# Kernel optimization log

Measured on AMD Instinct MI355X. Metric: run time of the kernel, lower is better.

Reference implementation:

```python
import jax, jax.numpy as jnp
import numpy as np

K = 16          # gcn_k
NHEAD = 4
C = 256         # feat_dims
EPS = 1e-5
LAYERS = ('gcn', 'cross_attn', 'gcn', 'cross_attn')


def _inorm(x, axes):
    # torch InstanceNorm (affine=False): normalize per (batch, channel) over spatial axes
    mu = jnp.mean(x, axes, keepdims=True)
    var = jnp.var(x, axes, keepdims=True)
    return (x - mu) * jax.lax.rsqrt(var + EPS)


def _lrelu(x):
    return jnp.where(x >= 0, x, 0.2 * x)


def _conv1d(x, W, b=None):
    # 1x1 Conv1d: x (B,Cin,N), W (Cout,Cin)
    y = jnp.einsum('bcn,oc->bon', x, W)
    return y if b is None else y + b[None, :, None]


def _graph_features(feats, coords, k):
    # feats (B,N,Cf), coords (B,N,3) -> (B,N,k,2Cf)  [EdgeConv features]
    sq = jnp.sum(coords * coords, axis=-1)  # (B,N)
    d = sq[:, :, None] + sq[:, None, :] - 2.0 * jnp.einsum('bnc,bmc->bnm', coords, coords)
    _, inds = jax.lax.top_k(-d, k + 1)       # k+1 smallest distances, sorted
    inds = inds[:, :, 1:]                    # drop self
    neigh = jax.vmap(lambda f, i: f[i])(feats, inds)  # (B,N,k,Cf)
    center = jnp.broadcast_to(feats[:, :, None, :], neigh.shape)
    return jnp.concatenate([center, neigh - center], axis=-1)


def _gcn(coords, feats, W1, W2, W3, k):
    # coords (B,3,N), feats (B,C,N) -> (B,C,N)
    c = jnp.transpose(coords, (0, 2, 1))
    f = jnp.transpose(feats, (0, 2, 1))
    g1 = _graph_features(f, c, k)                                   # (B,N,k,2C)
    h1 = _lrelu(_inorm(jnp.einsum('bnkc,oc->bonk', g1, W1), (2, 3)))
    f1 = jnp.max(h1, axis=-1)                                       # (B,C,N)
    g2 = _graph_features(jnp.transpose(f1, (0, 2, 1)), c, k)        # (B,N,k,2C)
    h2 = _lrelu(_inorm(jnp.einsum('bnkc,oc->bonk', g2, W2), (2, 3)))
    f2 = jnp.max(h2, axis=-1)                                       # (B,2C,N)
    f3 = jnp.concatenate([feats, f1, f2], axis=1)                   # (B,4C,N)
    return _lrelu(_inorm(_conv1d(f3, W3), (2,)))


def _cross_attn(f1, f2, Wq, bq, Wk, bk, Wv, bv, Wo, bo, Wm1, bm1, Wm2, bm2, nhead):
    B, Cc, N = f1.shape
    d = Cc // nhead
    # torch reshape (B, C, N) -> (B, d, nhead, N): channel c = dd*nhead + h
    q = _conv1d(f1, Wq, bq).reshape(B, d, nhead, -1)
    k = _conv1d(f2, Wk, bk).reshape(B, d, nhead, -1)
    v = _conv1d(f2, Wv, bv).reshape(B, d, nhead, -1)
    scores = jnp.einsum('bdhn,bdhm->bhnm', q, k) / (d ** 0.5)
    attn = jax.nn.softmax(scores, axis=-1)
    feats = jnp.einsum('bhnm,bdhm->bdhn', attn, v).reshape(B, Cc, -1)
    feats = _conv1d(feats, Wo, bo)
    h = _conv1d(jnp.concatenate([f1, feats], axis=1), Wm1, bm1)
    h = jax.nn.relu(_inorm(h, (2,)))
    return _conv1d(h, Wm2, bm2)


def _forward(coords1, feats1, coords2, feats2, gcn_W1, gcn_W2, gcn_W3, ca):
    for li, name in enumerate(LAYERS):
        i = li // 2  # index into stacked per-block params
        if name == 'gcn':
            feats1 = _gcn(coords1, feats1, gcn_W1[i], gcn_W2[i], gcn_W3[i], K)
            feats2 = _gcn(coords2, feats2, gcn_W1[i], gcn_W2[i], gcn_W3[i], K)
        else:
            p = tuple(t[i] for t in ca)
            feats1 = _cross_attn(feats1, feats2, *p, NHEAD)
            feats2 = _cross_attn(feats2, feats1, *p, NHEAD)
    return feats1, feats2


def setup_inputs() -> dict:
    key = jax.random.key(0)
    ks = jax.random.split(key, 20)
    B, N, M = 2, 2048, 2048
    s = 0.05
    f32 = jnp.float32
    return {
        'coords1': jax.random.normal(ks[0], (B, 3, N), f32),
        'feats1': jax.random.normal(ks[1], (B, C, N), f32),
        'coords2': jax.random.normal(ks[2], (B, 3, M), f32),
        'feats2': jax.random.normal(ks[3], (B, C, M), f32),
        'gcn_W1': jax.random.normal(ks[4], (2, C, 2 * C), f32) * s,
        'gcn_W2': jax.random.normal(ks[5], (2, 2 * C, 2 * C), f32) * s,
        'gcn_W3': jax.random.normal(ks[6], (2, C, 4 * C), f32) * s,
        'ca_Wq': jax.random.normal(ks[7], (2, C, C), f32) * s,
        'ca_bq': jax.random.normal(ks[8], (2, C), f32) * s,
        'ca_Wk': jax.random.normal(ks[9], (2, C, C), f32) * s,
        'ca_bk': jax.random.normal(ks[10], (2, C), f32) * s,
        'ca_Wv': jax.random.normal(ks[11], (2, C, C), f32) * s,
        'ca_bv': jax.random.normal(ks[12], (2, C), f32) * s,
        'ca_Wo': jax.random.normal(ks[13], (2, C, C), f32) * s,
        'ca_bo': jax.random.normal(ks[14], (2, C), f32) * s,
        'ca_Wm1': jax.random.normal(ks[15], (2, 2 * C, 2 * C), f32) * s,
        'ca_bm1': jax.random.normal(ks[16], (2, 2 * C), f32) * s,
        'ca_Wm2': jax.random.normal(ks[17], (2, C, 2 * C), f32) * s,
        'ca_bm2': jax.random.normal(ks[18], (2, C), f32) * s,
    }


def reference(coords1, feats1, coords2, feats2, gcn_W1, gcn_W2, gcn_W3,
              ca_Wq, ca_bq, ca_Wk, ca_bk, ca_Wv, ca_bv, ca_Wo, ca_bo,
              ca_Wm1, ca_bm1, ca_Wm2, ca_bm2):
    ca = (ca_Wq, ca_bq, ca_Wk, ca_bk, ca_Wv, ca_bv, ca_Wo, ca_bo,
          ca_Wm1, ca_bm1, ca_Wm2, ca_bm2)
    return _forward(coords1, feats1, coords2, feats2, gcn_W1, gcn_W2, gcn_W3, ca)
```

## Files before the change

### kernel.cpp

```cpp
#include <hip/hip_runtime.h>


namespace {

constexpr int BB = 2, NPV = 2048, CCH = 256, KNB = 16;
typedef long long i64;
typedef unsigned short u16;
constexpr i64 NSTR  = (i64)NPV * 256;
constexpr i64 NSTR2 = (i64)NPV * 512;
constexpr i64 NSTR4 = (i64)NPV * 1024;
constexpr i64 MB = 1048576;

typedef __attribute__((ext_vector_type(8))) short short8v;
typedef __attribute__((ext_vector_type(4))) float f32x4;

__device__ __forceinline__ float lrelu(float v) { return v >= 0.f ? v : 0.2f * v; }

__device__ __forceinline__ void splitbf(float x, u16& h, u16& l) {
  unsigned u = __float_as_uint(x);
  h = (u16)(u >> 16);
  float hf = __uint_as_float(u & 0xffff0000u);
  l = (u16)(__float_as_uint(x - hf) >> 16);
}

__global__ __launch_bounds__(256) void k_diag(float* out, int n, float v) {
  int i = blockIdx.x * 256 + threadIdx.x;
  if (i < n) out[i] = v;
}

__global__ __launch_bounds__(256) void k_setup(
    const float* __restrict__ fa, const float* __restrict__ fb,
    float* __restrict__ Xa, float* __restrict__ Xb,
    const float* __restrict__ W1b, const float* __restrict__ W2b,
    float* __restrict__ UVS,
    const float* __restrict__ Wob, float* __restrict__ WoT,
    const float* __restrict__ Wm1b_, float* __restrict__ Wfull,
    const float* __restrict__ bm1b_, const float* __restrict__ bob,
    float* __restrict__ bcomb) {
  int blk = blockIdx.x;
  int t = threadIdx.x;
  if (blk < 8192) {
    int gi = blk * 256 + t;
    bool second = gi >= (1 << 20);
    int idx = gi & ((1 << 20) - 1);
    int b = idx >> 19;
    int n = (idx >> 8) & (NPV - 1);
    int c = idx & (CCH - 1);
    const float* f = second ? fb : fa;
    float* X = second ? Xb : Xa;
    X[idx] = f[((i64)b * CCH + c) * NPV + n];
  } else if (blk < 11264) {
    int i = (blk - 8192) * 256 + t;
    int li = i / 393216;
    int r0 = i - li * 393216;
    const float* W1 = W1b + (i64)li * 131072;
    const float* W2 = W2b + (i64)li * 262144;
    float* dst = UVS + (i64)li * 393216;
    if (r0 < 131072) {
      int r = r0 >> 8, c = r0 & 255;
      dst[r0] = (r < 256) ? W1[(i64)r * 512 + c] - W1[(i64)r * 512 + 256 + c]
                          : W1[(i64)(r - 256) * 512 + 256 + c];
    } else {
      int j = r0 - 131072;
      int r = j >> 8, c = j & 255;
      dst[131072 + j] = (r < 512) ? W2[(i64)r * 512 + c] - W2[(i64)r * 512 + 256 + c]
                                  : W2[(i64)(r - 512) * 512 + 256 + c];
    }
  } else if (blk < 11776) {
    int i = (blk - 11264) * 256 + t;
    int li = i >> 16, rem = i & 65535;
    int c = rem >> 8, k = rem & 255;
    WoT[(i64)li * 65536 + c * 256 + k] = Wob[(i64)li * 65536 + k * 256 + c];
  } else if (blk < 12800) {
    int i = (blk - 11776) * 256 + t;
    int li = i >> 17, rem = i & 131071;
    int o = rem >> 8, c = rem & 255;
    Wfull[(i64)li * 262144 + o * 512 + c] = Wm1b_[(i64)li * 262144 + o * 512 + c];
  } else {
    int g = (blk - 12800) * 256 + t;
    int li = g >> 9, o = g & 511;
    const float* wm1 = Wm1b_ + (i64)li * 262144 + (i64)o * 512 + 256;
    const float* bo = bob + (i64)li * 256;
    float acc = bm1b_[(i64)li * 512 + o];
    for (int k = 0; k < 256; k++) acc += wm1[k] * bo[k];
    bcomb[(i64)li * 512 + o] = acc;
  }
}

__global__ __launch_bounds__(256) void k_final2(const float* __restrict__ Xa,
                                                const float* __restrict__ Xb,
                                                float* __restrict__ out) {
  int gi = blockIdx.x * 256 + threadIdx.x;
  bool second = gi >= (1 << 20);
  int idx = gi & ((1 << 20) - 1);
  int b = idx >> 19;
  int c = (idx >> 11) & (CCH - 1);
  int n = idx & (NPV - 1);
  const float* X = second ? Xb : Xa;
  out[gi] = X[((i64)b * NPV + n) * CCH + c];
}

__global__ __launch_bounds__(256) void k_knnp(const float* __restrict__ c1,
                                              const float* __restrict__ c2,
                                              int* __restrict__ o1,
                                              int* __restrict__ o2) {
#pragma clang fp contract(off)
  __shared__ float4 csq[NPV];
  int set = blockIdx.y >> 1, b = blockIdx.y & 1;
  const float* cb = (set ? c2 : c1) + (i64)b * 3 * NPV;
  int* ob = (set ? o2 : o1) + (i64)b * NPV * KNB;
  for (int m = threadIdx.x; m < NPV; m += 256) {
    float x = cb[m], y = cb[NPV + m], z = cb[2 * NPV + m];
    csq[m] = make_float4(x, y, z, x * x + y * y + z * z);
  }
  __syncthreads();
  int w = threadIdx.x >> 6, lane = threadIdx.x & 63;
  int n = blockIdx.x * 4 + w;
  float4 cn = csq[n];
  float xn = cn.x, yn = cn.y, zn = cn.z, sn = cn.w;
  float dc[32];
#pragma unroll
  for (int t = 0; t < 32; t++) {
    float4 c = csq[t * 64 + lane];
    float dot = xn * c.x + yn * c.y + zn * c.z;
    dc[t] = (sn + c.w) - 2.0f * dot;
  }
  float wd = -3.4e38f; int wm = -1;
  int* o = ob + (i64)n * KNB;
  for (int r = 0; r < KNB + 1; r++) {
    float bd = 3.4e38f; int bm = 0x7fffffff;
#pragma unroll
    for (int t = 0; t < 32; t++) {
      int m = t * 64 + lane;
      float d = dc[t];
      bool valid = (d > wd) || (d == wd && m > wm);
      if (valid && (d < bd || (d == bd && m < bm))) { bd = d; bm = m; }
    }
    for (int mask = 1; mask < 64; mask <<= 1) {
      float od = __shfl_xor(bd, mask);
      int om = __shfl_xor(bm, mask);
      if (od < bd || (od == bd && om < bm)) { bd = od; bm = om; }
    }
    if (r > 0 && lane == 0) o[r - 1] = bm & (NPV - 1);
    wd = bd; wm = bm;
  }
}

template <bool ANORM, bool ACAT, bool ESTAT>
__global__ __launch_bounds__(256) void k_gemm(
    const float* __restrict__ A, int lda, i64 sA,
    const float* __restrict__ A2,
    const float* __restrict__ W, int ldw, i64 sW,
    const float* __restrict__ bias,
    float* __restrict__ C, int ldc, i64 sC,
    int K, int mode, int act,
    const float* __restrict__ pin, int nchA, float invA,
    float* __restrict__ pout, int ncolsTot) {
  __shared__ __align__(16) u16 Ah[128][36], Al[128][36], Bh[128][36], Bl[128][36];
  __shared__ float mv[512], rv[512];
  __shared__ float cs[128][2];
  int b = blockIdx.z;
  A += (i64)b * sA;
  if (ACAT) A2 += (i64)b * NSTR;
  C += (i64)b * sC;
  int m0 = blockIdx.x * 128, n0 = blockIdx.y * 128;
  int tid = threadIdx.x;
  int w = tid >> 6, l = tid & 63;
  int wr = w >> 1, wc = w & 1;
  int lc = l & 15, lq = l >> 4;
  int srow = tid >> 1, skh = (tid & 1) * 16;

  if (ANORM) {
    for (int c = tid; c < K; c += 256) {
      float s = 0.f, ss = 0.f;
      for (int hh = 0; hh < nchA; hh++) {
        s  += pin[((i64)(b * nchA + hh) * K + c) * 2];
        ss += pin[((i64)(b * nchA + hh) * K + c) * 2 + 1];
      }
      float mu = s * invA;
      mv[c] = mu;
      rv[c] = 1.0f / sqrtf(ss * invA - mu * mu + 1e-5f);
    }
    __syncthreads();
  }

  const float* Ap = A + (i64)(m0 + srow) * lda + skh;
  const float* Wp = W + (i64)b * sW + (i64)(n0 + srow) * ldw + skh;

  auto loadA = [&](int kt, float4* v) {
#pragma unroll
    for (int j = 0; j < 4; j++) {
      if (ACAT) {
        int col0 = kt + skh;
        const float* ap = (col0 < 256)
            ? A  + (i64)(m0 + srow) * 256 + col0
            : A2 + (i64)(m0 + srow) * 256 + (col0 - 256);
        v[j] = *(const float4*)(ap + j * 4);
      } else {
        v[j] = *(const float4*)(Ap + kt + j * 4);
      }
    }
  };
  auto loadW = [&](int kt, float4* v) {
#pragma unroll
    for (int j = 0; j < 4; j++) v[j] = *(const float4*)(Wp + kt + j * 4);
  };

  float4 ar[4], wv4[4];
  loadA(0, ar); loadW(0, wv4);

  f32x4 acc[4][4];
#pragma unroll
  for (int i = 0; i < 4; i++)
#pragma unroll
    for (int j = 0; j < 4; j++)
#pragma unroll
      for (int r = 0; r < 4; r++) acc[i][j][r] = 0.f;

  int koff = lq * 8;
  for (int kt = 0; kt < K; kt += 32) {
    __syncthreads();
#pragma unroll
    for (int j = 0; j < 4; j++) {
      float4 a = ar[j];
      if (ANORM) {
        float4 mu = *(const float4*)&mv[kt + skh + j * 4];
        float4 rs = *(const float4*)&rv[kt + skh + j * 4];
        a.x = (a.x - mu.x) * rs.x; a.y = (a.y - mu.y) * rs.y;
        a.z = (a.z - mu.z) * rs.z; a.w = (a.w - mu.w) * rs.w;
        if (act == 1) { a.x = lrelu(a.x); a.y = lrelu(a.y);
                        a.z = lrelu(a.z); a.w = lrelu(a.w); }
        else { a.x = fmaxf(a.x, 0.f); a.y = fmaxf(a.y, 0.f);
               a.z = fmaxf(a.z, 0.f); a.w = fmaxf(a.w, 0.f); }
      }
      u16 h0, h1, h2, h3, l0, l1, l2, l3;
      splitbf(a.x, h0, l0); splitbf(a.y, h1, l1);
      splitbf(a.z, h2, l2); splitbf(a.w, h3, l3);
      *(ushort4*)&Ah[srow][skh + j * 4] = make_ushort4(h0, h1, h2, h3);
      *(ushort4*)&Al[srow][skh + j * 4] = make_ushort4(l0, l1, l2, l3);
      float4 bb = wv4[j];
      splitbf(bb.x, h0, l0); splitbf(bb.y, h1, l1);
      splitbf(bb.z, h2, l2); splitbf(bb.w, h3, l3);
      *(ushort4*)&Bh[srow][skh + j * 4] = make_ushort4(h0, h1, h2, h3);
      *(ushort4*)&Bl[srow][skh + j * 4] = make_ushort4(l0, l1, l2, l3);
    }
    __syncthreads();
    if (kt + 32 < K) { loadA(kt + 32, ar); loadW(kt + 32, wv4); }
    short8v ah[4], al4[4], bh[4], bl4[4];
#pragma unroll
    for (int i = 0; i < 4; i++) {
      int r = wr * 64 + i * 16 + lc;
      ah[i]  = *(const short8v*)&Ah[r][koff];
      al4[i] = *(const short8v*)&Al[r][koff];
    }
#pragma unroll
    for (int j = 0; j < 4; j++) {
      int r = wc * 64 + j * 16 + lc;
      bh[j]  = *(const short8v*)&Bh[r][koff];
      bl4[j] = *(const short8v*)&Bl[r][koff];
    }
#pragma unroll
    for (int i = 0; i < 4; i++) {
#pragma unroll
      for (int j = 0; j < 4; j++) {
        acc[i][j] = __builtin_amdgcn_mfma_f32_16x16x32_bf16(ah[i], bh[j], acc[i][j], 0, 0, 0);
        acc[i][j] = __builtin_amdgcn_mfma_f32_16x16x32_bf16(al4[i], bh[j], acc[i][j], 0, 0, 0);
        acc[i][j] = __builtin_amdgcn_mfma_f32_16x16x32_bf16(ah[i], bl4[j], acc[i][j], 0, 0, 0);
      }
    }
  }

  float sj[4] = {0.f, 0.f, 0.f, 0.f}, ssj[4] = {0.f, 0.f, 0.f, 0.f};
#pragma unroll
  for (int j = 0; j < 4; j++) {
    int col = n0 + wc * 64 + j * 16 + lc;
    float bv = (mode == 0 && bias) ? bias[col] : 0.f;
#pragma unroll
    for (int i = 0; i < 4; i++) {
      int rbase = m0 + wr * 64 + i * 16 + lq * 4;
#pragma unroll
      for (int r = 0; r < 4; r++) {
        float* cp = &C[(i64)(rbase + r) * ldc + col];
        float v = acc[i][j][r] + ((mode == 0) ? bv : *cp);
        *cp = v;
        if (ESTAT) { sj[j] += v; ssj[j] += v * v; }
      }
    }
  }
  if (ESTAT) {
#pragma unroll
    for (int j = 0; j < 4; j++) {
      sj[j]  += __shfl_xor(sj[j], 16);  sj[j]  += __shfl_xor(sj[j], 32);
      ssj[j] += __shfl_xor(ssj[j], 16); ssj[j] += __shfl_xor(ssj[j], 32);
    }
    __syncthreads();
    if (wr == 0 && lq == 0) {
#pragma unroll
      for (int j = 0; j < 4; j++) {
        int cl = wc * 64 + j * 16 + lc;
        cs[cl][0] = sj[j]; cs[cl][1] = ssj[j];
      }
    }
    __syncthreads();
    if (wr == 1 && lq == 0) {
#pragma unroll
      for (int j = 0; j < 4; j++) {
        int cl = wc * 64 + j * 16 + lc;
        cs[cl][0] += sj[j]; cs[cl][1] += ssj[j];
      }
    }
    __syncthreads();
    if (tid < 128) {
      i64 slot = ((i64)(b * gridDim.x + blockIdx.x) * ncolsTot + n0 + tid) * 2;
      pout[slot] = cs[tid][0];
      pout[slot + 1] = cs[tid][1];
    }
  }
}

__global__ __launch_bounds__(256) void k_qkv(
    const float* __restrict__ XA, const float* __restrict__ XB,
    const float* __restrict__ Wq, const float* __restrict__ Wk,
    const float* __restrict__ Wv,
    const float* __restrict__ bq, const float* __restrict__ bk,
    const float* __restrict__ bv,
    float* __restrict__ Qp, float* __restrict__ Kp, float* __restrict__ Vp) {
  __shared__ __align__(16) u16 Ah[128][36], Al[128][36], Bh[128][36], Bl[128][36];
  int z = blockIdx.z;
  int mat = z >> 1, b = z & 1;
  const float* A = (mat == 0 ? XA : XB) + (i64)b * NSTR;
  const float* W = (mat == 0 ? Wq : (mat == 1 ? Wk : Wv));
  const float* bias = (mat == 0 ? bq : (mat == 1 ? bk : bv));
  float* C = (mat == 0 ? Qp : (mat == 1 ? Kp : Vp)) + (i64)b * NSTR;
  int m0 = blockIdx.x * 128, n0 = blockIdx.y * 128;
  int tid = threadIdx.x;
  int w = tid >> 6, l = tid & 63;
  int wr = w >> 1, wc = w & 1;
  int lc = l & 15, lq = l >> 4;
  int srow = tid >> 1, skh = (tid & 1) * 16;
  const float* Ap = A + (i64)(m0 + srow) * 256 + skh;
  const float* Wp = W + (i64)(n0 + srow) * 256 + skh;
  float4 ar[4], wv4[4];
#pragma unroll
  for (int j = 0; j < 4; j++) { ar[j] = *(const float4*)(Ap + j * 4);
                                wv4[j] = *(const float4*)(Wp + j * 4); }
  f32x4 acc[4][4];
#pragma unroll
  for (int i = 0; i < 4; i++)
#pragma unroll
    for (int j = 0; j < 4; j++)
#pragma unroll
      for (int r = 0; r < 4; r++) acc[i][j][r] = 0.f;
  int koff = lq * 8;
  for (int kt = 0; kt < 256; kt += 32) {
    __syncthreads();
#pragma unroll
    for (int j = 0; j < 4; j++) {
      u16 h0, h1, h2, h3, l0, l1, l2, l3;
      splitbf(ar[j].x, h0, l0); splitbf(ar[j].y, h1, l1);
      splitbf(ar[j].z, h2, l2); splitbf(ar[j].w, h3, l3);
      *(ushort4*)&Ah[srow][skh + j * 4] = make_ushort4(h0, h1, h2, h3);
      *(ushort4*)&Al[srow][skh + j * 4] = make_ushort4(l0, l1, l2, l3);
      splitbf(wv4[j].x, h0, l0); splitbf(wv4[j].y, h1, l1);
      splitbf(wv4[j].z, h2, l2); splitbf(wv4[j].w, h3, l3);
      *(ushort4*)&Bh[srow][skh + j * 4] = make_ushort4(h0, h1, h2, h3);
      *(ushort4*)&Bl[srow][skh + j * 4] = make_ushort4(l0, l1, l2, l3);
    }
    __syncthreads();
    if (kt + 32 < 256) {
#pragma unroll
      for (int j = 0; j < 4; j++) { ar[j] = *(const float4*)(Ap + kt + 32 + j * 4);
                                    wv4[j] = *(const float4*)(Wp + kt + 32 + j * 4); }
    }
    short8v ah[4], al4[4], bh[4], bl4[4];
#pragma unroll
    for (int i = 0; i < 4; i++) {
      int r = wr * 64 + i * 16 + lc;
      ah[i]  = *(const short8v*)&Ah[r][koff];
      al4[i] = *(const short8v*)&Al[r][koff];
    }
#pragma unroll
    for (int j = 0; j < 4; j++) {
      int r = wc * 64 + j * 16 + lc;
      bh[j]  = *(const short8v*)&Bh[r][koff];
      bl4[j] = *(const short8v*)&Bl[r][koff];
    }
#pragma unroll
    for (int i = 0; i < 4; i++)
#pragma unroll
      for (int j = 0; j < 4; j++) {
        acc[i][j] = __builtin_amdgcn_mfma_f32_16x16x32_bf16(ah[i], bh[j], acc[i][j], 0, 0, 0);
        acc[i][j] = __builtin_amdgcn_mfma_f32_16x16x32_bf16(al4[i], bh[j], acc[i][j], 0, 0, 0);
        acc[i][j] = __builtin_amdgcn_mfma_f32_16x16x32_bf16(ah[i], bl4[j], acc[i][j], 0, 0, 0);
      }
  }
#pragma unroll
  for (int j = 0; j < 4; j++) {
    int col = n0 + wc * 64 + j * 16 + lc;
    float bv = bias[col];
#pragma unroll
    for (int i = 0; i < 4; i++) {
      int rbase = m0 + wr * 64 + i * 16 + lq * 4;
#pragma unroll
      for (int r = 0; r < 4; r++) {
        float v = acc[i][j][r] + bv;
        int row = rbase + r;
        if (mat == 0) C[(i64)row * 256 + col] = v;
        else C[((i64)(col & 3) * 2048 + row) * 64 + (col >> 2)] = v;
      }
    }
  }
}

__global__ __launch_bounds__(256) void k_y3(
    const float* __restrict__ Xbase, const float* __restrict__ F1b,
    const float* __restrict__ F2b, const float* __restrict__ W3b,
    float* __restrict__ Cb,
    const float* __restrict__ pA, const float* __restrict__ pB,
    float* __restrict__ pout, int li) {
  __shared__ __align__(16) u16 Ah[128][36], Al[128][36], Bh[128][36], Bl[128][36];
  __shared__ float mv[1024], rv[1024];
  __shared__ float cs[128][2];
  int z = blockIdx.z;
  const float* X = Xbase + (i64)z * NSTR;
  const float* F1 = F1b + (i64)z * NSTR;
  const float* F2 = F2b + (i64)z * NSTR2;
  const float* W3 = W3b + (i64)li * 262144;
  float* C = Cb + (i64)z * NSTR;
  int m0 = blockIdx.x * 128, n0 = blockIdx.y * 128;
  int tid = threadIdx.x;
  int w = tid >> 6, l = tid & 63;
  int wr = w >> 1, wc = w & 1;
  int lc = l & 15, lq = l >> 4;
  int srow = tid >> 1, skh = (tid & 1) * 16;
  for (int c = tid; c < 768; c += 256) {
    int col = 256 + c;
    const float* P; int cols, idx;
    if (col < 512) { P = pA; cols = 256; idx = col - 256; }
    else           { P = pB; cols = 512; idx = col - 512; }
    float s = 0.f, ss = 0.f;
    for (int hh = 0; hh < 64; hh++) {
      s  += P[((i64)(z * 64 + hh) * cols + idx) * 2];
      ss += P[((i64)(z * 64 + hh) * cols + idx) * 2 + 1];
    }
    float mu = s * (1.f / 32768.f);
    mv[col] = mu;
    rv[col] = 1.0f / sqrtf(ss * (1.f / 32768.f) - mu * mu + 1e-5f);
  }
  __syncthreads();
  auto loadA = [&](int kt, float4* v) {
    int col0 = kt + skh;
    const float* ap;
    if (col0 < 256)      ap = X  + (i64)(m0 + srow) * 256 + col0;
    else if (col0 < 512) ap = F1 + (i64)(m0 + srow) * 256 + (col0 - 256);
    else                 ap = F2 + (i64)(m0 + srow) * 512 + (col0 - 512);
#pragma unroll
    for (int j = 0; j < 4; j++) v[j] = *(const float4*)(ap + j * 4);
  };
  const float* Wp = W3 + (i64)(n0 + srow) * 1024 + skh;
  float4 ar[4], wv4[4];
  loadA(0, ar);
#pragma unroll
  for (int j = 0; j < 4; j++) wv4[j] = *(const float4*)(Wp + j * 4);
  f32x4 acc[4][4];
#pragma unroll
  for (int i = 0; i < 4; i++)
#pragma unroll
    for (int j = 0; j < 4; j++)
#pragma unroll
      for (int r = 0; r < 4; r++) acc[i][j][r] = 0.f;
  int koff = lq * 8;
  for (int kt = 0; kt < 1024; kt += 32) {
    __syncthreads();
    int col0 = kt + skh;
#pragma unroll
    for (int j = 0; j < 4; j++) {
      float4 a = ar[j];
      if (col0 >= 256) {
        float4 mu = *(const float4*)&mv[col0 + j * 4];
        float4 rs = *(const float4*)&rv[col0 + j * 4];
        a.x = lrelu((a.x - mu.x) * rs.x);
        a.y = lrelu((a.y - mu.y) * rs.y);
        a.z = lrelu((a.z - mu.z) * rs.z);
        a.w = lrelu((a.w - mu.w) * rs.w);
      }
      u16 h0, h1, h2, h3, l0, l1, l2, l3;
      splitbf(a.x, h0, l0); splitbf(a.y, h1, l1);
      splitbf(a.z, h2, l2); splitbf(a.w, h3, l3);
      *(ushort4*)&Ah[srow][skh + j * 4] = make_ushort4(h0, h1, h2, h3);
      *(ushort4*)&Al[srow][skh + j * 4] = make_ushort4(l0, l1, l2, l3);
      splitbf(wv4[j].x, h0, l0); splitbf(wv4[j].y, h1, l1);
      splitbf(wv4[j].z, h2, l2); splitbf(wv4[j].w, h3, l3);
      *(ushort4*)&Bh[srow][skh + j * 4] = make_ushort4(h0, h1, h2, h3);
      *(ushort4*)&Bl[srow][skh + j * 4] = make_ushort4(l0, l1, l2, l3);
    }
    __syncthreads();
    if (kt + 32 < 1024) {
      loadA(kt + 32, ar);
#pragma unroll
      for (int j = 0; j < 4; j++) wv4[j] = *(const float4*)(Wp + kt + 32 + j * 4);
    }
    short8v ah[4], al4[4], bh[4], bl4[4];
#pragma unroll
    for (int i = 0; i < 4; i++) {
      int r = wr * 64 + i * 16 + lc;
      ah[i]  = *(const short8v*)&Ah[r][koff];
      al4[i] = *(const short8v*)&Al[r][koff];
    }
#pragma unroll
    for (int j = 0; j < 4; j++) {
      int r = wc * 64 + j * 16 + lc;
      bh[j]  = *(const short8v*)&Bh[r][koff];
      bl4[j] = *(const short8v*)&Bl[r][koff];
    }
#pragma unroll
    for (int i = 0; i < 4; i++)
#pragma unroll
      for (int j = 0; j < 4; j++) {
        acc[i][j] = __builtin_amdgcn_mfma_f32_16x16x32_bf16(ah[i], bh[j], acc[i][j], 0, 0, 0);
        acc[i][j] = __builtin_amdgcn_mfma_f32_16x16x32_bf16(al4[i], bh[j], acc[i][j], 0, 0, 0);
        acc[i][j] = __builtin_amdgcn_mfma_f32_16x16x32_bf16(ah[i], bl4[j], acc[i][j], 0, 0, 0);
      }
  }
  float sj[4] = {0.f, 0.f, 0.f, 0.f}, ssj[4] = {0.f, 0.f, 0.f, 0.f};
#pragma unroll
  for (int j = 0; j < 4; j++) {
    int col = n0 + wc * 64 + j * 16 + lc;
#pragma unroll
    for (int i = 0; i < 4; i++) {
      int rbase = m0 + wr * 64 + i * 16 + lq * 4;
#pragma unroll
      for (int r = 0; r < 4; r++) {
        float v = acc[i][j][r];
        C[(i64)(rbase + r) * 256 + col] = v;
        sj[j] += v; ssj[j] += v * v;
      }
    }
  }
#pragma unroll
  for (int j = 0; j < 4; j++) {
    sj[j]  += __shfl_xor(sj[j], 16);  sj[j]  += __shfl_xor(sj[j], 32);
    ssj[j] += __shfl_xor(ssj[j], 16); ssj[j] += __shfl_xor(ssj[j], 32);
  }
  __syncthreads();
  if (wr == 0 && lq == 0) {
#pragma unroll
    for (int j = 0; j < 4; j++) {
      int cl = wc * 64 + j * 16 + lc;
      cs[cl][0] = sj[j]; cs[cl][1] = ssj[j];
    }
  }
  __syncthreads();
  if (wr == 1 && lq == 0) {
#pragma unroll
    for (int j = 0; j < 4; j++) {
      int cl = wc * 64 + j * 16 + lc;
      cs[cl][0] += sj[j]; cs[cl][1] += ssj[j];
    }
  }
  __syncthreads();
  if (tid < 128) {
    i64 slot = ((i64)(z * 16 + blockIdx.x) * 256 + n0 + tid) * 2;
    pout[slot] = cs[tid][0];
    pout[slot + 1] = cs[tid][1];
  }
}

__global__ __launch_bounds__(256) void k_gstat(const float* __restrict__ P,
                                               const float* __restrict__ Q,
                                               int ldpq,
                                               const int* __restrict__ knn,
                                               int O, float* __restrict__ RM,
                                               float* __restrict__ part) {
  int b = blockIdx.z;
  int o = blockIdx.x * 256 + threadIdx.x;
  int n0 = blockIdx.y * 32;
  P += (i64)b * 2048 * ldpq; Q += (i64)b * 2048 * ldpq; RM += (i64)b * 2048 * O;
  knn += ((i64)b * 2048 + n0) * KNB;
  __shared__ int js[32 * KNB];
  for (int i = threadIdx.x; i < 32 * KNB; i += 256) js[i] = knn[i];
  __syncthreads();
  float s = 0.f, ss = 0.f;
  for (int r = 0; r < 32; r++) {
    int n = n0 + r;
    float p = P[(i64)n * ldpq + o];
    float qm = -3.4e38f, qs = 0.f, qss = 0.f;
#pragma unroll
    for (int k = 0; k < KNB; k++) {
      float q = Q[(i64)js[r * KNB + k] * ldpq + o];
      qm = fmaxf(qm, q); qs += q; qss += q * q;
    }
    RM[(i64)n * O + o] = p + qm;
    s  += 16.f * p + qs;
    ss += 16.f * p * p + 2.f * p * qs + qss;
  }
  i64 slot = ((i64)b * 64 + blockIdx.y) * O + o;
  part[slot * 2] = s; part[slot * 2 + 1] = ss;
}

__global__ __launch_bounds__(256) void k_normP(const float* __restrict__ src,
                                               float* __restrict__ dst, int cols,
                                               const float* __restrict__ part,
                                               int nch, float inv, int act) {
  int b = blockIdx.z;
  i64 n = blockIdx.x;
  int c = blockIdx.y * 256 + threadIdx.x;
  float s = 0.f, ss = 0.f;
  for (int h = 0; h < nch; h++) {
    s  += part[((i64)(b * nch + h) * cols + c) * 2];
    ss += part[((i64)(b * nch + h) * cols + c) * 2 + 1];
  }
  float mu = s * inv;
  float rs = 1.0f / sqrtf(ss * inv - mu * mu + 1e-5f);
  i64 off = ((i64)b * 2048 + n) * cols + c;
  float v = (src[off] - mu) * rs;
  dst[off] = (act == 1) ? lrelu(v) : fmaxf(v, 0.f);
}

__global__ __launch_bounds__(256) void k_flash(const float* __restrict__ Qp,
                                               const float* __restrict__ Kp,
                                               const float* __restrict__ Vp,
                                               float* __restrict__ Op) {
  __shared__ __align__(16) u16 Kh[64][76], Kl[64][76];
  __shared__ __align__(16) u16 Vh[64][76], Vl[64][76];
  __shared__ __align__(16) u16 Ph[4][16][76], Pl[4][16][76];
  int qt = blockIdx.x, h = blockIdx.y, b = blockIdx.z;
  const float* Qb = Qp + (i64)b * NSTR;
  const float* Khm = Kp + (i64)b * NSTR + (i64)h * 131072;
  const float* Vhm = Vp + (i64)b * NSTR + (i64)h * 131072;
  int tid = threadIdx.x;
  int w = tid >> 6, l = tid & 63;
  int lc = l & 15, lq = l >> 4;
  short8v qh[2], ql[2];
  int qrow = qt * 64 + w * 16 + lc;
#pragma unroll
  for (int ks = 0; ks < 2; ks++) {
#pragma unroll
    for (int j = 0; j < 8; j++) {
      float v = Qb[(i64)qrow * 256 + 4 * (ks * 32 + lq * 8 + j) + h];
      u16 hh, ll; splitbf(v, hh, ll);
      qh[ks][j] = (short)hh; ql[ks][j] = (short)ll;
    }
  }
  float m_r[4] = {-3.0e38f, -3.0e38f, -3.0e38f, -3.0e38f};
  float l_r[4] = {0.f, 0.f, 0.f, 0.f};
  f32x4 acc[4];
#pragma unroll
  for (int j = 0; j < 4; j++)
#pragma unroll
    for (int r = 0; r < 4; r++) acc[j][r] = 0.f;

  for (int kt = 0; kt < 32; kt++) {
    __syncthreads();
    {
      const float* Kt = Khm + (i64)kt * 4096;
      const float* Vt = Vhm + (i64)kt * 4096;
#pragma unroll
      for (int q = 0; q < 4; q++) {
        int v = q * 256 + tid;
        int m = v >> 4, d4 = (v & 15) * 4;
        u16 h0, h1, h2, h3, l0, l1, l2, l3;
        float4 kf = *(const float4*)(Kt + (i64)v * 4);
        splitbf(kf.x, h0, l0); splitbf(kf.y, h1, l1);
        splitbf(kf.z, h2, l2); splitbf(kf.w, h3, l3);
        *(ushort4*)&Kh[m][d4] = make_ushort4(h0, h1, h2, h3);
        *(ushort4*)&Kl[m][d4] = make_ushort4(l0, l1, l2, l3);
        float4 vf = *(const float4*)(Vt + (i64)v * 4);
        splitbf(vf.x, h0, l0); splitbf(vf.y, h1, l1);
        splitbf(vf.z, h2, l2); splitbf(vf.w, h3, l3);
        Vh[d4 + 0][m] = h0; Vh[d4 + 1][m] = h1;
        Vh[d4 + 2][m] = h2; Vh[d4 + 3][m] = h3;
        Vl[d4 + 0][m] = l0; Vl[d4 + 1][m] = l1;
        Vl[d4 + 2][m] = l2; Vl[d4 + 3][m] = l3;
      }
    }
    __syncthreads();
    f32x4 s[4];
#pragma unroll
    for (int j = 0; j < 4; j++)
#pragma unroll
      for (int r = 0; r < 4; r++) s[j][r] = 0.f;
#pragma unroll
    for (int ks = 0; ks < 2; ks++) {
      int ko = ks * 32 + lq * 8;
#pragma unroll
      for (int j = 0; j < 4; j++) {
        short8v bh = *(const short8v*)&Kh[j * 16 + lc][ko];
        short8v bl = *(const short8v*)&Kl[j * 16 + lc][ko];
        s[j] = __builtin_amdgcn_mfma_f32_16x16x32_bf16(qh[ks], bh, s[j], 0, 0, 0);
        s[j] = __builtin_amdgcn_mfma_f32_16x16x32_bf16(ql[ks], bh, s[j], 0, 0, 0);
        s[j] = __builtin_amdgcn_mfma_f32_16x16x32_bf16(qh[ks], bl, s[j], 0, 0, 0);
      }
    }
#pragma unroll
    for (int j = 0; j < 4; j++)
#pragma unroll
      for (int r = 0; r < 4; r++) s[j][r] *= 0.125f;
    float rmax[4];
#pragma unroll
    for (int r = 0; r < 4; r++)
      rmax[r] = fmaxf(fmaxf(s[0][r], s[1][r]), fmaxf(s[2][r], s[3][r]));
#pragma unroll
    for (int mask = 1; mask < 16; mask <<= 1)
#pragma unroll
      for (int r = 0; r < 4; r++) rmax[r] = fmaxf(rmax[r], __shfl_xor(rmax[r], mask));
    float fs[4], rsum[4];
#pragma unroll
    for (int r = 0; r < 4; r++) {
      float mn = fmaxf(m_r[r], rmax[r]);
      fs[r] = expf(m_r[r] - mn);
      m_r[r] = mn; rsum[r] = 0.f;
    }
#pragma unroll
    for (int j = 0; j < 4; j++)
#pragma unroll
      for (int r = 0; r < 4; r++) {
        float p = expf(s[j][r] - m_r[r]);
        rsum[r] += p;
        u16 hh, ll; splitbf(p, hh, ll);
        Ph[w][lq * 4 + r][j * 16 + lc] = hh;
        Pl[w][lq * 4 + r][j * 16 + lc] = ll;
      }
#pragma unroll
    for (int mask = 1; mask < 16; mask <<= 1)
#pragma unroll
      for (int r = 0; r < 4; r++) rsum[r] += __shfl_xor(rsum[r], mask);
#pragma unroll
    for (int r = 0; r < 4; r++) l_r[r] = l_r[r] * fs[r] + rsum[r];
#pragma unroll
    for (int j = 0; j < 4; j++)
#pragma unroll
      for (int r = 0; r < 4; r++) acc[j][r] *= fs[r];
#pragma unroll
    for (int ks = 0; ks < 2; ks++) {
      int ko = ks * 32 + lq * 8;
      short8v ph = *(const short8v*)&Ph[w][lc][ko];
      short8v pl = *(const short8v*)&Pl[w][lc][ko];
#pragma unroll
      for (int j = 0; j < 4; j++) {
        short8v bh = *(const short8v*)&Vh[j * 16 + lc][ko];
        short8v bl = *(const short8v*)&Vl[j * 16 + lc][ko];
        acc[j] = __builtin_amdgcn_mfma_f32_16x16x32_bf16(ph, bh, acc[j], 0, 0, 0);
        acc[j] = __builtin_amdgcn_mfma_f32_16x16x32_bf16(pl, bh, acc[j], 0, 0, 0);
        acc[j] = __builtin_amdgcn_mfma_f32_16x16x32_bf16(ph, bl, acc[j], 0, 0, 0);
      }
    }
  }
  float* Ob = Op + (i64)b * NSTR;
#pragma unroll
  for (int j = 0; j < 4; j++) {
    int dd = j * 16 + lc;
#pragma unroll
    for (int r = 0; r < 4; r++) {
      int q = qt * 64 + w * 16 + lq * 4 + r;
      Ob[(i64)q * 256 + 4 * dd + h] = acc[j][r] / l_r[r];
    }
  }
}

}

extern "C" void kernel_launch(void* const* d_in, const int* in_sizes, int n_in,
                              void* d_out, int out_size, void* d_ws, size_t ws_size,
                              hipStream_t stream) {
  float* outp = (float*)d_out;
  auto diag = [&](float v) {
    k_diag<<<dim3((out_size + 255) / 256), dim3(256), 0, stream>>>(outp, out_size, v);
  };

  static const int DSZ[19] = {12288, 1048576, 12288, 1048576, 262144, 524288, 524288,
                              131072, 512, 131072, 512, 131072, 512, 131072, 512,
                              524288, 1024, 262144, 512};
  if (n_in != 19) { diag(1000.f + (float)n_in); return; }
  for (int i = 0; i < 19; i++) {
    if (in_sizes[i] != DSZ[i]) { diag(2000.f + (float)i); return; }
  }
  if (out_size != 2097152) { diag(3000.f); return; }
  constexpr size_t NEED = 50331648;
  if (ws_size < NEED) { diag((float)(ws_size >> 20)); return; }

  char* w = (char*)d_ws;
  float* S0 = (float*)(w + 0);
  float* S1 = (float*)(w + 4 * MB);
  int*   KN1 = (int*)(w + 8 * MB);
  int*   KN2 = (int*)(w + 8 * MB + 262144);
  float* PARTA = (float*)(w + 8912896);
  float* PARTB = (float*)(w + 9437184);
  float* PARTCg = (float*)(w + 10485760);
  float* PARTCa = (float*)(w + 10616832);
  float* BCOMB = (float*)(w + 10747904);
  float* UVS   = (float*)(w + 10752000);
  float* WFULL = (float*)(w + 13897728);
  float* WOT   = (float*)(w + 15994880);
  char* AR = w + 16519168;

  float* PQ1 = (float*)(AR);
  float* PQ2 = (float*)(AR);
  float* F2  = (float*)(AR + 16 * MB);
  float* Y3  = (float*)(AR);
  float* F1d = (float*)d_out;
  float* Qp = (float*)(AR);
  float* Kp = (float*)(AR + 4 * MB);
  float* Vp = (float*)(AR + 8 * MB);
  float* Oc = (float*)(AR + 12 * MB);
  float* Hh = (float*)(AR + 16 * MB);

  const float* W1b = (const float*)d_in[4];
  const float* W2b = (const float*)d_in[5];
  const float* W3b = (const float*)d_in[6];
  const float* Wqb = (const float*)d_in[7];   const float* bqb = (const float*)d_in[8];
  const float* Wkb = (const float*)d_in[9];   const float* bkb = (const float*)d_in[10];
  const float* Wvb = (const float*)d_in[11];  const float* bvb = (const float*)d_in[12];
  const float* Wob = (const float*)d_in[13];  const float* bob = (const float*)d_in[14];
  const float* Wm1b = (const float*)d_in[15]; const float* bm1b = (const float*)d_in[16];
  const float* Wm2b = (const float*)d_in[17]; const float* bm2b = (const float*)d_in[18];

  k_knnp<<<dim3(NPV / 4, 4), dim3(256), 0, stream>>>((const float*)d_in[0],
                                                     (const float*)d_in[2], KN1, KN2);
  k_setup<<<dim3(12804), dim3(256), 0, stream>>>(
      (const float*)d_in[1], (const float*)d_in[3], S0, S1,
      W1b, W2b, UVS, Wob, WOT, Wm1b, WFULL, bm1b, bob, BCOMB);
  k_gemm<false, false, false><<<dim3(4, 2, 2), dim3(256), 0, stream>>>(
      Wm1b + 256, 512, 262144, nullptr, WOT, 256, 65536, nullptr,
      WFULL + 256, 512, 262144, 256, 0, 0, nullptr, 0, 0.f, nullptr, 0);

  auto gcn = [&](int li) {
    const float* UV1 = UVS + (i64)li * 393216;
    const float* UV2 = UVS + (i64)li * 393216 + 131072;
    k_gemm<false, false, false><<<dim3(16, 4, 4), dim3(256), 0, stream>>>(
        S0, 256, NSTR, nullptr, UV1, 256, 0, nullptr, PQ1, 512, NSTR2, 256, 0, 0,
        nullptr, 0, 0.f, nullptr, 0);
    k_gstat<<<dim3(1, 64, 4), dim3(256), 0, stream>>>(PQ1, PQ1 + 256, 512, KN1,
                                                      256, F1d, PARTA);
    for (int s = 0; s < 2; s++) {
      k_gemm<true, false, false><<<dim3(16, 8, 2), dim3(256), 0, stream>>>(
          F1d + (i64)s * 2 * NSTR, 256, NSTR, nullptr, UV2, 256, 0, nullptr,
          PQ2, 1024, NSTR4, 256, 0, 1,
          PARTA + (i64)s * 65536, 64, 1.f / 32768.f, nullptr, 0);
      k_gstat<<<dim3(2, 64, 2), dim3(256), 0, stream>>>(
          PQ2, PQ2 + 512, 1024, KN1 + (i64)s * 65536,
          512, F2 + (i64)s * 2 * NSTR2, PARTB + (i64)s * 131072);
    }
    k_y3<<<dim3(16, 2, 4), dim3(256), 0, stream>>>(S0, F1d, F2, W3b, Y3,
                                                   PARTA, PARTB, PARTCg, li);
    k_normP<<<dim3(2048, 1, 4), dim3(256), 0, stream>>>(Y3, S0, 256, PARTCg, 16,
                                                        1.f / 2048.f, 1);
  };

  auto attn = [&](const float* XA, const float* XB, float* XO, int li) {
    const float* Wq = Wqb + (i64)li * 65536;   const float* bq = bqb + (i64)li * 256;
    const float* Wk = Wkb + (i64)li * 65536;   const float* bk = bkb + (i64)li * 256;
    const float* Wv = Wvb + (i64)li * 65536;   const float* bv = bvb + (i64)li * 256;
    const float* Wm2 = Wm2b + (i64)li * 131072; const float* bm2 = bm2b + (i64)li * 256;
    k_qkv<<<dim3(16, 2, 6), dim3(256), 0, stream>>>(XA, XB, Wq, Wk, Wv,
                                                    bq, bk, bv, Qp, Kp, Vp);
    k_flash<<<dim3(32, 4, BB), dim3(256), 0, stream>>>(Qp, Kp, Vp, Oc);
    k_gemm<false, true, true><<<dim3(16, 4, 2), dim3(256), 0, stream>>>(
        XA, 256, NSTR, Oc, WFULL + (i64)li * 262144, 512, 0,
        BCOMB + (i64)li * 512, Hh, 512, NSTR2, 512, 0, 0,
        nullptr, 0, 0.f, PARTCa, 512);
    k_gemm<true, false, false><<<dim3(16, 2, 2), dim3(256), 0, stream>>>(
        Hh, 512, NSTR2, nullptr, Wm2, 512, 0, bm2, XO, 256, NSTR, 512, 0, 2,
        PARTCa, 16, 1.f / 2048.f, nullptr, 0);
  };

  gcn(0);
  attn(S0, S1, S0, 0);
  attn(S1, S0, S1, 0);
  gcn(1);
  attn(S0, S1, S0, 1);
  attn(S1, S0, S1, 1);

  k_final2<<<dim3(8192), dim3(256), 0, stream>>>(S0, S1, outp);
}
```

Measured before the change: 1.643 ms.

## Split kNN across warps, store PQ2 in bf16, merge gcn loop, fuse final transpose

The kNN kernel now gives each point a whole block: four warps each take a quarter of the candidates and a final warp merges their sorted top-17 lists, which raises parallelism. The second gcn GEMM writes its PQ2 output as round-to-nearest bf16, and k_gstat reads it as bf16. This halves the gather traffic and lets the two half-batch GEMM/gstat pairs become one launch each over the full batch. The final transpose kernel is removed, and the last attention GEMMs write the transposed output directly. The bf16 storage of the pre-norm features lowers precision in the max/stat path.

```diff
diff --git a/kernel.cpp b/kernel.cpp
--- a/kernel.cpp
+++ b/kernel.cpp
@@ -6,6 +6,7 @@
 constexpr int BB = 2, NPV = 2048, CCH = 256, KNB = 16;
 typedef long long i64;
 typedef unsigned short u16;
+typedef unsigned int u32;
 constexpr i64 NSTR  = (i64)NPV * 256;
 constexpr i64 NSTR2 = (i64)NPV * 512;
 constexpr i64 NSTR4 = (i64)NPV * 1024;
@@ -21,6 +22,14 @@
   h = (u16)(u >> 16);
   float hf = __uint_as_float(u & 0xffff0000u);
   l = (u16)(__float_as_uint(x - hf) >> 16);
+}
+
+__device__ __forceinline__ u16 f2bf_rn(float x) {
+  u32 u = __float_as_uint(x);
+  return (u16)((u + 0x7fffu + ((u >> 16) & 1u)) >> 16);
+}
+__device__ __forceinline__ float bf2f(u16 h) {
+  return __uint_as_float((u32)h << 16);
 }
 
 __global__ __launch_bounds__(256) void k_diag(float* out, int n, float v) {
@@ -87,51 +96,40 @@
   }
 }
 
-__global__ __launch_bounds__(256) void k_final2(const float* __restrict__ Xa,
-                                                const float* __restrict__ Xb,
-                                                float* __restrict__ out) {
-  int gi = blockIdx.x * 256 + threadIdx.x;
-  bool second = gi >= (1 << 20);
-  int idx = gi & ((1 << 20) - 1);
-  int b = idx >> 19;
-  int c = (idx >> 11) & (CCH - 1);
-  int n = idx & (NPV - 1);
-  const float* X = second ? Xb : Xa;
-  out[gi] = X[((i64)b * NPV + n) * CCH + c];
-}
-
 __global__ __launch_bounds__(256) void k_knnp(const float* __restrict__ c1,
                                               const float* __restrict__ c2,
                                               int* __restrict__ o1,
                                               int* __restrict__ o2) {
 #pragma clang fp contract(off)
   __shared__ float4 csq[NPV];
+  __shared__ float md[4 * 17];
+  __shared__ int   mi[4 * 17];
   int set = blockIdx.y >> 1, b = blockIdx.y & 1;
   const float* cb = (set ? c2 : c1) + (i64)b * 3 * NPV;
   int* ob = (set ? o2 : o1) + (i64)b * NPV * KNB;
-  for (int m = threadIdx.x; m < NPV; m += 256) {
+  int tid = threadIdx.x;
+  for (int m = tid; m < NPV; m += 256) {
     float x = cb[m], y = cb[NPV + m], z = cb[2 * NPV + m];
     csq[m] = make_float4(x, y, z, x * x + y * y + z * z);
   }
   __syncthreads();
-  int w = threadIdx.x >> 6, lane = threadIdx.x & 63;
-  int n = blockIdx.x * 4 + w;
+  int w = tid >> 6, lane = tid & 63;
+  int n = blockIdx.x;
   float4 cn = csq[n];
   float xn = cn.x, yn = cn.y, zn = cn.z, sn = cn.w;
-  float dc[32];
-#pragma unroll
-  for (int t = 0; t < 32; t++) {
-    float4 c = csq[t * 64 + lane];
+  float dc[8];
+#pragma unroll
+  for (int t = 0; t < 8; t++) {
+    float4 c = csq[w * 512 + t * 64 + lane];
     float dot = xn * c.x + yn * c.y + zn * c.z;
     dc[t] = (sn + c.w) - 2.0f * dot;
   }
   float wd = -3.4e38f; int wm = -1;
-  int* o = ob + (i64)n * KNB;
   for (int r = 0; r < KNB + 1; r++) {
     float bd = 3.4e38f; int bm = 0x7fffffff;
 #pragma unroll
-    for (int t = 0; t < 32; t++) {
-      int m = t * 64 + lane;
+    for (int t = 0; t < 8; t++) {
+      int m = w * 512 + t * 64 + lane;
       float d = dc[t];
       bool valid = (d > wd) || (d == wd && m > wm);
       if (valid && (d < bd || (d == bd && m < bm))) { bd = d; bm = m; }
@@ -141,12 +139,33 @@
       int om = __shfl_xor(bm, mask);
       if (od < bd || (od == bd && om < bm)) { bd = od; bm = om; }
     }
-    if (r > 0 && lane == 0) o[r - 1] = bm & (NPV - 1);
+    if (lane == 0) { md[w * 17 + r] = bd; mi[w * 17 + r] = bm; }
     wd = bd; wm = bm;
   }
-}
-
-template <bool ANORM, bool ACAT, bool ESTAT>
+  __syncthreads();
+  if (w == 0) {
+    int ptr = 0;
+    float hd = (lane < 4) ? md[lane * 17] : 3.4e38f;
+    int   hm = (lane < 4) ? mi[lane * 17] : 0x7fffffff;
+    int* o = ob + (i64)n * KNB;
+    for (int r = 0; r < KNB + 1; r++) {
+      float bd = hd; int bm = hm;
+      for (int mask = 1; mask < 64; mask <<= 1) {
+        float od = __shfl_xor(bd, mask);
+        int om = __shfl_xor(bm, mask);
+        if (od < bd || (od == bd && om < bm)) { bd = od; bm = om; }
+      }
+      if (r > 0 && lane == 0) o[r - 1] = bm & (NPV - 1);
+      if (lane < 4 && hd == bd && hm == bm) {
+        ptr++;
+        hd = (ptr < 17) ? md[lane * 17 + ptr] : 3.4e38f;
+        hm = (ptr < 17) ? mi[lane * 17 + ptr] : 0x7fffffff;
+      }
+    }
+  }
+}
+
+template <bool ANORM, bool ACAT, bool ESTAT, int OMODE>
 __global__ __launch_bounds__(256) void k_gemm(
     const float* __restrict__ A, int lda, i64 sA,
     const float* __restrict__ A2,
@@ -155,14 +174,14 @@
     float* __restrict__ C, int ldc, i64 sC,
     int K, int mode, int act,
     const float* __restrict__ pin, int nchA, float invA,
-    float* __restrict__ pout, int ncolsTot) {
+    float* __restrict__ pout, int ncolsTot,
+    int tmode, float* __restrict__ out2) {
   __shared__ __align__(16) u16 Ah[128][36], Al[128][36], Bh[128][36], Bl[128][36];
   __shared__ float mv[512], rv[512];
   __shared__ float cs[128][2];
   int b = blockIdx.z;
   A += (i64)b * sA;
   if (ACAT) A2 += (i64)b * NSTR;
-  C += (i64)b * sC;
   int m0 = blockIdx.x * 128, n0 = blockIdx.y * 128;
   int tid = threadIdx.x;
   int w = tid >> 6, l = tid & 63;
@@ -280,9 +299,18 @@
       int rbase = m0 + wr * 64 + i * 16 + lq * 4;
 #pragma unroll
       for (int r = 0; r < 4; r++) {
-        float* cp = &C[(i64)(rbase + r) * ldc + col];
-        float v = acc[i][j][r] + ((mode == 0) ? bv : *cp);
-        *cp = v;
+        int row = rbase + r;
+        float v;
+        if (OMODE == 1) {
+          v = acc[i][j][r];
+          ((u16*)C)[(i64)b * sC + (i64)row * ldc + col] = f2bf_rn(v);
+        } else {
+          float* cp = &C[(i64)b * sC + (i64)row * ldc + col];
+          v = acc[i][j][r] + ((mode == 0) ? bv : *cp);
+          if (tmode != 2) *cp = v;
+          if (tmode != 0)
+            out2[(i64)b * 524288 + (i64)col * 2048 + row] = v;
+        }
         if (ESTAT) { sj[j] += v; ssj[j] += v * v; }
       }
     }
@@ -566,8 +594,9 @@
   }
 }
 
-__global__ __launch_bounds__(256) void k_gstat(const float* __restrict__ P,
-                                               const float* __restrict__ Q,
+template <bool BF16IN>
+__global__ __launch_bounds__(256) void k_gstat(const void* __restrict__ Pv,
+                                               const void* __restrict__ Qv,
                                                int ldpq,
                                                const int* __restrict__ knn,
                                                int O, float* __restrict__ RM,
@@ -575,19 +604,22 @@
   int b = blockIdx.z;
   int o = blockIdx.x * 256 + threadIdx.x;
   int n0 = blockIdx.y * 32;
-  P += (i64)b * 2048 * ldpq; Q += (i64)b * 2048 * ldpq; RM += (i64)b * 2048 * O;
+  RM += (i64)b * 2048 * O;
   knn += ((i64)b * 2048 + n0) * KNB;
   __shared__ int js[32 * KNB];
   for (int i = threadIdx.x; i < 32 * KNB; i += 256) js[i] = knn[i];
   __syncthreads();
+  i64 base = (i64)b * 2048 * ldpq;
   float s = 0.f, ss = 0.f;
   for (int r = 0; r < 32; r++) {
     int n = n0 + r;
-    float p = P[(i64)n * ldpq + o];
+    float p = BF16IN ? bf2f(((const u16*)Pv)[base + (i64)n * ldpq + o])
+                     : ((const float*)Pv)[base + (i64)n * ldpq + o];
     float qm = -3.4e38f, qs = 0.f, qss = 0.f;
 #pragma unroll
     for (int k = 0; k < KNB; k++) {
-      float q = Q[(i64)js[r * KNB + k] * ldpq + o];
+      i64 qoff = base + (i64)js[r * KNB + k] * ldpq + o;
+      float q = BF16IN ? bf2f(((const u16*)Qv)[qoff]) : ((const float*)Qv)[qoff];
       qm = fmaxf(qm, q); qs += q; qss += q * q;
     }
     RM[(i64)n * O + o] = p + qm;
@@ -791,11 +823,11 @@
   float* BCOMB = (float*)(w + 10747904);
   float* UVS   = (float*)(w + 10752000);
   float* WFULL = (float*)(w + 13897728);
-  float* WOT   = (float*)(w + 15994880);
-  char* AR = w + 16519168;
-
+  char* AR = w + 15994880;
+
+  float* WOT = (float*)(AR + 24 * MB);
   float* PQ1 = (float*)(AR);
-  float* PQ2 = (float*)(AR);
+  u16*   PQ2 = (u16*)(AR);
   float* F2  = (float*)(AR + 16 * MB);
   float* Y3  = (float*)(AR);
   float* F1d = (float*)d_out;
@@ -815,39 +847,38 @@
   const float* Wm1b = (const float*)d_in[15]; const float* bm1b = (const float*)d_in[16];
   const float* Wm2b = (const float*)d_in[17]; const float* bm2b = (const float*)d_in[18];
 
-  k_knnp<<<dim3(NPV / 4, 4), dim3(256), 0, stream>>>((const float*)d_in[0],
-                                                     (const float*)d_in[2], KN1, KN2);
+  k_knnp<<<dim3(NPV, 4), dim3(256), 0, stream>>>((const float*)d_in[0],
+                                                 (const float*)d_in[2], KN1, KN2);
   k_setup<<<dim3(12804), dim3(256), 0, stream>>>(
       (const float*)d_in[1], (const float*)d_in[3], S0, S1,
       W1b, W2b, UVS, Wob, WOT, Wm1b, WFULL, bm1b, bob, BCOMB);
-  k_gemm<false, false, false><<<dim3(4, 2, 2), dim3(256), 0, stream>>>(
+  k_gemm<false, false, false, 0><<<dim3(4, 2, 2), dim3(256), 0, stream>>>(
       Wm1b + 256, 512, 262144, nullptr, WOT, 256, 65536, nullptr,
-      WFULL + 256, 512, 262144, 256, 0, 0, nullptr, 0, 0.f, nullptr, 0);
+      WFULL + 256, 512, 262144, 256, 0, 0, nullptr, 0, 0.f, nullptr, 0,
+      0, nullptr);
 
   auto gcn = [&](int li) {
     const float* UV1 = UVS + (i64)li * 393216;
     const float* UV2 = UVS + (i64)li * 393216 + 131072;
-    k_gemm<false, false, false><<<dim3(16, 4, 4), dim3(256), 0, stream>>>(
+    k_gemm<false, false, false, 0><<<dim3(16, 4, 4), dim3(256), 0, stream>>>(
         S0, 256, NSTR, nullptr, UV1, 256, 0, nullptr, PQ1, 512, NSTR2, 256, 0, 0,
-        nullptr, 0, 0.f, nullptr, 0);
-    k_gstat<<<dim3(1, 64, 4), dim3(256), 0, stream>>>(PQ1, PQ1 + 256, 512, KN1,
-                                                      256, F1d, PARTA);
-    for (int s = 0; s < 2; s++) {
-      k_gemm<true, false, false><<<dim3(16, 8, 2), dim3(256), 0, stream>>>(
-          F1d + (i64)s * 2 * NSTR, 256, NSTR, nullptr, UV2, 256, 0, nullptr,
-          PQ2, 1024, NSTR4, 256, 0, 1,
-          PARTA + (i64)s * 65536, 64, 1.f / 32768.f, nullptr, 0);
-      k_gstat<<<dim3(2, 64, 2), dim3(256), 0, stream>>>(
-          PQ2, PQ2 + 512, 1024, KN1 + (i64)s * 65536,
-          512, F2 + (i64)s * 2 * NSTR2, PARTB + (i64)s * 131072);
-    }
+        nullptr, 0, 0.f, nullptr, 0, 0, nullptr);
+    k_gstat<false><<<dim3(1, 64, 4), dim3(256), 0, stream>>>(
+        PQ1, PQ1 + 256, 512, KN1, 256, F1d, PARTA);
+    k_gemm<true, false, false, 1><<<dim3(16, 8, 4), dim3(256), 0, stream>>>(
+        F1d, 256, NSTR, nullptr, UV2, 256, 0, nullptr,
+        (float*)PQ2, 1024, NSTR4, 256, 0, 1,
+        PARTA, 64, 1.f / 32768.f, nullptr, 0, 0, nullptr);
+    k_gstat<true><<<dim3(2, 64, 4), dim3(256), 0, stream>>>(
+        PQ2, PQ2 + 512, 1024, KN1, 512, F2, PARTB);
     k_y3<<<dim3(16, 2, 4), dim3(256), 0, stream>>>(S0, F1d, F2, W3b, Y3,
                                                    PARTA, PARTB, PARTCg, li);
     k_normP<<<dim3(2048, 1, 4), dim3(256), 0, stream>>>(Y3, S0, 256, PARTCg, 16,
                                                         1.f / 2048.f, 1);
   };
 
-  auto attn = [&](const float* XA, const float* XB, float* XO, int li) {
+  auto attn = [&](const float* XA, const float* XB, float* XO, int li,
+                  int tmode, float* out2) {
     const float* Wq = Wqb + (i64)li * 65536;   const float* bq = bqb + (i64)li * 256;
     const float* Wk = Wkb + (i64)li * 65536;   const float* bk = bkb + (i64)li * 256;
     const float* Wv = Wvb + (i64)li * 65536;   const float* bv = bvb + (i64)li * 256;
@@ -855,21 +886,19 @@
     k_qkv<<<dim3(16, 2, 6), dim3(256), 0, stream>>>(XA, XB, Wq, Wk, Wv,
                                                     bq, bk, bv, Qp, Kp, Vp);
     k_flash<<<dim3(32, 4, BB), dim3(256), 0, stream>>>(Qp, Kp, Vp, Oc);
-    k_gemm<false, true, true><<<dim3(16, 4, 2), dim3(256), 0, stream>>>(
+    k_gemm<false, true, true, 0><<<dim3(16, 4, 2), dim3(256), 0, stream>>>(
         XA, 256, NSTR, Oc, WFULL + (i64)li * 262144, 512, 0,
         BCOMB + (i64)li * 512, Hh, 512, NSTR2, 512, 0, 0,
-        nullptr, 0, 0.f, PARTCa, 512);
-    k_gemm<true, false, false><<<dim3(16, 2, 2), dim3(256), 0, stream>>>(
+        nullptr, 0, 0.f, PARTCa, 512, 0, nullptr);
+    k_gemm<true, false, false, 0><<<dim3(16, 2, 2), dim3(256), 0, stream>>>(
         Hh, 512, NSTR2, nullptr, Wm2, 512, 0, bm2, XO, 256, NSTR, 512, 0, 2,
-        PARTCa, 16, 1.f / 2048.f, nullptr, 0);
+        PARTCa, 16, 1.f / 2048.f, nullptr, 0, tmode, out2);
   };
 
   gcn(0);
-  attn(S0, S1, S0, 0);
-  attn(S1, S0, S1, 0);
+  attn(S0, S1, S0, 0, 0, nullptr);
+  attn(S1, S0, S1, 0, 0, nullptr);
   gcn(1);
-  attn(S0, S1, S0, 1);
-  attn(S1, S0, S1, 1);
-
-  k_final2<<<dim3(8192), dim3(256), 0, stream>>>(S0, S1, outp);
-}
+  attn(S0, S1, S0, 1, 1, outp);
+  attn(S1, S0, S1, 1, 2, outp + 1048576);
+}
```

Result: faster. 1.574 ms (-4.2%).
